# Optimization experiments

Measured on AMD Instinct MI355X. Metric: run time of the kernel, lower is better.

The kernel has to match this reference:

```python
import jax, jax.numpy as jnp
import numpy as np


def setup_inputs() -> dict:
    key = jax.random.key(0)
    k1, k2, k3, k4, k5, k6 = jax.random.split(key, 6)
    N, D, K = 8192, 1024, 64
    return {
        "x1": jax.random.normal(k1, (N, D), dtype=jnp.float32),
        "x2": jax.random.normal(k2, (1, D), dtype=jnp.float32),
        "V": jax.random.normal(k3, (K, 2 * D), dtype=jnp.float32) * 0.02,
        "W": jax.random.normal(k4, (K, D, D), dtype=jnp.float32) * 0.02,
        "b": jax.random.normal(k5, (K,), dtype=jnp.float32),
        "U": jax.random.normal(k6, (K, 1), dtype=jnp.float32) * 0.1,
    }


def reference(x1, x2, V, W, b, U):
    # x1: (N, D), x2: (1, D)
    # V term: per slice i, [x1 | tile(x2)] @ V[i] -> fused as one GEMM (N, K)
    cat = jnp.concatenate([x1, jnp.broadcast_to(x2, x1.shape)], axis=1)  # (N, 2D)
    v_term = cat @ V.T  # (N, K)
    # W bilinear term: x1 @ W[i] @ x2^T for each i. Contract x2 into W first
    # (K*D*D flops) then one (N,D)x(D,K) GEMM -- same math, efficient order.
    Wx2 = jnp.einsum('kde,e->kd', W, x2[0])  # (K, D)
    w_term = x1 @ Wx2.T  # (N, K)
    feat = jax.nn.relu(v_term + w_term + b)  # (N, K)
    return feat @ U  # (N, 1)
```

## Files before the change

kernel.cpp:

```cpp
#include <hip/hip_runtime.h>

#define D 1024
#define K 64
#define NROWS 8192

__global__ __launch_bounds__(256) void k1_wx2(
    const float* __restrict__ W, const float* __restrict__ V,
    const float* __restrict__ x2, const float* __restrict__ b,
    float* __restrict__ M, float* __restrict__ c) {
  __shared__ float xsh[D];
  int t = threadIdx.x;
  ((float4*)xsh)[t] = ((const float4*)x2)[t];
  __syncthreads();

  int lane = t & 63;
  int wv = t >> 6;
  long row = (long)blockIdx.x * 4 + wv;
  const long WROWS = (long)K * D;

  const float* src;
  bool is_w = (row < WROWS);
  if (is_w) {
    src = W + row * D;
  } else {
    long k = row - WROWS;
    if (k >= K) return;
    src = V + k * (2 * D) + D;
  }

  const float4* s4 = (const float4*)src;
  const float4* x4 = (const float4*)xsh;
  float sum = 0.f;
#pragma unroll
  for (int it = 0; it < 4; ++it) {
    float4 w = s4[lane + it * 64];
    float4 xv = x4[lane + it * 64];
    sum += w.x * xv.x + w.y * xv.y + w.z * xv.z + w.w * xv.w;
  }
#pragma unroll
  for (int off = 32; off; off >>= 1) sum += __shfl_down(sum, off, 64);

  if (lane == 0) {
    if (is_w) {
      long k = row >> 10;
      long d = row & (D - 1);
      M[row] = sum + V[k * (2 * D) + d];
    } else {
      long k = row - WROWS;
      c[k] = sum + b[k];
    }
  }
}

template <int NSPLIT>
__global__ __launch_bounds__(256, 3) void k2_gemm(
    const float* __restrict__ x1, const float* __restrict__ M,
    float* __restrict__ p) {
  __shared__ float xs[16][256];
  __shared__ float ms[16][64];
  int t = threadIdx.x;
  int nt = blockIdx.x / NSPLIT;
  int sp = blockIdx.x % NSPLIT;
  const int DSP = D / NSPLIT;
  const int NIT = DSP / 16;
  int n0 = nt * 256;
  int d0 = sp * DSP;

  int tx = t & 7;
  int ty = t >> 3;
  int mk = t & 63;
  int mg = t >> 6;

  const float4* xrow = (const float4*)(x1 + (long)(n0 + t) * D + d0);
  const float4* mrow = (const float4*)(M + (long)mk * D + d0) + mg;

  float acc[8][8];
#pragma unroll
  for (int i = 0; i < 8; ++i)
#pragma unroll
    for (int j = 0; j < 8; ++j) acc[i][j] = 0.f;

  float4 xreg[4], mreg;
#pragma unroll
  for (int h = 0; h < 4; ++h) xreg[h] = xrow[h];
  mreg = mrow[0];

#pragma unroll 1
  for (int it = 0; it < NIT; ++it) {
#pragma unroll
    for (int h = 0; h < 4; ++h) {
      xs[h * 4 + 0][t] = xreg[h].x;
      xs[h * 4 + 1][t] = xreg[h].y;
      xs[h * 4 + 2][t] = xreg[h].z;
      xs[h * 4 + 3][t] = xreg[h].w;
    }
    ms[mg * 4 + 0][mk] = mreg.x;
    ms[mg * 4 + 1][mk] = mreg.y;
    ms[mg * 4 + 2][mk] = mreg.z;
    ms[mg * 4 + 3][mk] = mreg.w;
    __syncthreads();

    if (it + 1 < NIT) {
#pragma unroll
      for (int h = 0; h < 4; ++h) xreg[h] = xrow[(it + 1) * 4 + h];
      mreg = mrow[(it + 1) * 4];
    }

#pragma unroll
    for (int d = 0; d < 16; ++d) {
      float4 a0 = *(const float4*)&xs[d][ty * 8];
      float4 a1 = *(const float4*)&xs[d][ty * 8 + 4];
      float4 b0 = *(const float4*)&ms[d][tx * 8];
      float4 b1 = *(const float4*)&ms[d][tx * 8 + 4];
      float xa[8] = {a0.x, a0.y, a0.z, a0.w, a1.x, a1.y, a1.z, a1.w};
      float mb[8] = {b0.x, b0.y, b0.z, b0.w, b1.x, b1.y, b1.z, b1.w};
#pragma unroll
      for (int i = 0; i < 8; ++i)
#pragma unroll
        for (int j = 0; j < 8; ++j)
          acc[i][j] = fmaf(xa[i], mb[j], acc[i][j]);
    }
    __syncthreads();
  }

  float* dst = p + ((long)sp * NROWS + n0 + (long)ty * 8) * K + tx * 8;
#pragma unroll
  for (int i = 0; i < 8; ++i) {
    float4 v0 = {acc[i][0], acc[i][1], acc[i][2], acc[i][3]};
    float4 v1 = {acc[i][4], acc[i][5], acc[i][6], acc[i][7]};
    *(float4*)&dst[(long)i * K] = v0;
    *(float4*)&dst[(long)i * K + 4] = v1;
  }
}

template <int NSPLIT>
__global__ __launch_bounds__(256) void k3_reduce(
    const float* __restrict__ p, const float* __restrict__ c,
    const float* __restrict__ U, float* __restrict__ out) {
  int t = threadIdx.x;
  int lane = t & 63;
  int n = blockIdx.x * 4 + (t >> 6);
  float s = 0.f;
#pragma unroll
  for (int sp = 0; sp < NSPLIT; ++sp)
    s += p[((long)sp * NROWS + n) * K + lane];
  float v = fmaxf(s + c[lane], 0.f) * U[lane];
#pragma unroll
  for (int off = 32; off; off >>= 1) v += __shfl_down(v, off, 64);
  if (lane == 0) out[n] = v;
}

extern "C" void kernel_launch(void* const* d_in, const int* in_sizes, int n_in,
                              void* d_out, int out_size, void* d_ws, size_t ws_size,
                              hipStream_t stream) {
  const float* x1 = (const float*)d_in[0];
  const float* x2 = (const float*)d_in[1];
  const float* V = (const float*)d_in[2];
  const float* W = (const float*)d_in[3];
  const float* b = (const float*)d_in[4];
  const float* U = (const float*)d_in[5];
  float* out = (float*)d_out;

  float* M = (float*)d_ws;
  float* c = M + (long)K * D;
  float* partial = c + 64;

  k1_wx2<<<dim3(16400), dim3(256), 0, stream>>>(W, V, x2, b, M, c);

  size_t need8 = (size_t)(K * D + 64 + 8L * NROWS * K) * sizeof(float);
  if (ws_size >= need8) {
    k2_gemm<8><<<dim3(256), dim3(256), 0, stream>>>(x1, M, partial);
    k3_reduce<8><<<dim3(NROWS / 4), dim3(256), 0, stream>>>(partial, c, U, out);
  } else {
    k2_gemm<1><<<dim3(32), dim3(256), 0, stream>>>(x1, M, partial);
    k3_reduce<1><<<dim3(NROWS / 4), dim3(256), 0, stream>>>(partial, c, U, out);
  }
}
```

Before: 398.9 us.

## Reduce split-K partials with float atomics and use nontemporal streaming loads

The split-K GEMM now accumulates into a single N×K buffer with unsafeAtomicAdd, replacing the eight partial slabs that the reduce kernel had to read back. The first kernel zeroes that buffer. Loads of W and x1 are switched to nontemporal loads so this single-use streaming data does not pollute the caches. This removes about 16MB of partial writes and reads and simplifies the final kernel, in exchange for many atomic operations and a nondeterministic summation order.

Measured after the change: 484.7 us. +21.5%, slower.

```diff
diff --git a/kernel.cpp b/kernel.cpp
--- a/kernel.cpp
+++ b/kernel.cpp
@@ -4,12 +4,18 @@
 #define K 64
 #define NROWS 8192
 
+typedef float nf4 __attribute__((ext_vector_type(4)));
+
+
 __global__ __launch_bounds__(256) void k1_wx2(
     const float* __restrict__ W, const float* __restrict__ V,
     const float* __restrict__ x2, const float* __restrict__ b,
-    float* __restrict__ M, float* __restrict__ c) {
+    float* __restrict__ M, float* __restrict__ c, float* __restrict__ s) {
   __shared__ float xsh[D];
   int t = threadIdx.x;
+
+  if (blockIdx.x < (NROWS * K / 256)) s[(long)blockIdx.x * 256 + t] = 0.f;
+
   ((float4*)xsh)[t] = ((const float4*)x2)[t];
   __syncthreads();
 
@@ -28,12 +34,12 @@
     src = V + k * (2 * D) + D;
   }
 
-  const float4* s4 = (const float4*)src;
+  const nf4* s4 = (const nf4*)src;
   const float4* x4 = (const float4*)xsh;
   float sum = 0.f;
 #pragma unroll
   for (int it = 0; it < 4; ++it) {
-    float4 w = s4[lane + it * 64];
+    nf4 w = __builtin_nontemporal_load(&s4[lane + it * 64]);
     float4 xv = x4[lane + it * 64];
     sum += w.x * xv.x + w.y * xv.y + w.z * xv.z + w.w * xv.w;
   }
@@ -55,7 +61,7 @@
 template <int NSPLIT>
 __global__ __launch_bounds__(256, 3) void k2_gemm(
     const float* __restrict__ x1, const float* __restrict__ M,
-    float* __restrict__ p) {
+    float* __restrict__ s) {
   __shared__ float xs[16][256];
   __shared__ float ms[16][64];
   int t = threadIdx.x;
@@ -71,7 +77,7 @@
   int mk = t & 63;
   int mg = t >> 6;
 
-  const float4* xrow = (const float4*)(x1 + (long)(n0 + t) * D + d0);
+  const nf4* xrow = (const nf4*)(x1 + (long)(n0 + t) * D + d0);
   const float4* mrow = (const float4*)(M + (long)mk * D + d0) + mg;
 
   float acc[8][8];
@@ -80,9 +86,10 @@
 #pragma unroll
     for (int j = 0; j < 8; ++j) acc[i][j] = 0.f;
 
-  float4 xreg[4], mreg;
+  nf4 xreg[4];
+  float4 mreg;
 #pragma unroll
-  for (int h = 0; h < 4; ++h) xreg[h] = xrow[h];
+  for (int h = 0; h < 4; ++h) xreg[h] = __builtin_nontemporal_load(&xrow[h]);
   mreg = mrow[0];
 
 #pragma unroll 1
@@ -102,7 +109,8 @@
 
     if (it + 1 < NIT) {
 #pragma unroll
-      for (int h = 0; h < 4; ++h) xreg[h] = xrow[(it + 1) * 4 + h];
+      for (int h = 0; h < 4; ++h)
+        xreg[h] = __builtin_nontemporal_load(&xrow[(it + 1) * 4 + h]);
       mreg = mrow[(it + 1) * 4];
     }
 
@@ -123,28 +131,21 @@
     __syncthreads();
   }
 
-  float* dst = p + ((long)sp * NROWS + n0 + (long)ty * 8) * K + tx * 8;
+  float* dst = s + (long)(n0 + ty * 8) * K + tx * 8;
 #pragma unroll
-  for (int i = 0; i < 8; ++i) {
-    float4 v0 = {acc[i][0], acc[i][1], acc[i][2], acc[i][3]};
-    float4 v1 = {acc[i][4], acc[i][5], acc[i][6], acc[i][7]};
-    *(float4*)&dst[(long)i * K] = v0;
-    *(float4*)&dst[(long)i * K + 4] = v1;
-  }
+  for (int i = 0; i < 8; ++i)
+#pragma unroll
+    for (int j = 0; j < 8; ++j)
+      unsafeAtomicAdd(&dst[(long)i * K + j], acc[i][j]);
 }
 
-template <int NSPLIT>
-__global__ __launch_bounds__(256) void k3_reduce(
-    const float* __restrict__ p, const float* __restrict__ c,
+__global__ __launch_bounds__(256) void k3_final(
+    const float* __restrict__ s, const float* __restrict__ c,
     const float* __restrict__ U, float* __restrict__ out) {
   int t = threadIdx.x;
   int lane = t & 63;
   int n = blockIdx.x * 4 + (t >> 6);
-  float s = 0.f;
-#pragma unroll
-  for (int sp = 0; sp < NSPLIT; ++sp)
-    s += p[((long)sp * NROWS + n) * K + lane];
-  float v = fmaxf(s + c[lane], 0.f) * U[lane];
+  float v = fmaxf(s[(long)n * K + lane] + c[lane], 0.f) * U[lane];
 #pragma unroll
   for (int off = 32; off; off >>= 1) v += __shfl_down(v, off, 64);
   if (lane == 0) out[n] = v;
@@ -163,16 +164,11 @@
 
   float* M = (float*)d_ws;
   float* c = M + (long)K * D;
-  float* partial = c + 64;
+  float* s = c + 64;
 
-  k1_wx2<<<dim3(16400), dim3(256), 0, stream>>>(W, V, x2, b, M, c);
+  k1_wx2<<<dim3(16400), dim3(256), 0, stream>>>(W, V, x2, b, M, c, s);
 
-  size_t need8 = (size_t)(K * D + 64 + 8L * NROWS * K) * sizeof(float);
-  if (ws_size >= need8) {
-    k2_gemm<8><<<dim3(256), dim3(256), 0, stream>>>(x1, M, partial);
-    k3_reduce<8><<<dim3(NROWS / 4), dim3(256), 0, stream>>>(partial, c, U, out);
-  } else {
-    k2_gemm<1><<<dim3(32), dim3(256), 0, stream>>>(x1, M, partial);
-    k3_reduce<1><<<dim3(NROWS / 4), dim3(256), 0, stream>>>(partial, c, U, out);
-  }
+  k2_gemm<8><<<dim3(256), dim3(256), 0, stream>>>(x1, M, s);
+
+  k3_final<<<dim3(NROWS / 4), dim3(256), 0, stream>>>(s, c, U, out);
 }
```
